# Kernel tuning notes

Measured on AMD Instinct MI355X. Metric: run time of the kernel, lower is better.

The kernel has to match this reference:

```python
import jax, jax.numpy as jnp
import numpy as np

D_MODEL, D_STATE, D_CONV, EXPAND = 1024, 16, 4, 2
D_INNER = EXPAND * D_MODEL
DT_RANK = (D_MODEL + 15) // 16  # 64
B_SZ, SEQ = 2, 1024


def _mamba_dir(x, inW, convW, convB, xpW, dtW, dtB, Alog, Dp, outW):
    """Standard Mamba block forward. x: [B, L, d_model]."""
    Bsz, L, _ = x.shape
    d_inner, d_state = Alog.shape
    dt_rank = xpW.shape[0] - 2 * d_state
    xz = jnp.einsum('bld,ed->ble', x, inW)            # [B, L, 2*d_inner]
    xi, z = jnp.split(xz, 2, axis=-1)
    # depthwise causal conv along L
    xc = jnp.swapaxes(xi, 1, 2)                       # [B, d_inner, L]
    xc = jax.lax.conv_general_dilated(
        xc, convW, window_strides=(1,),
        padding=[(convW.shape[-1] - 1, 0)],
        feature_group_count=d_inner)
    xc = xc + convB[None, :, None]
    u = jax.nn.silu(jnp.swapaxes(xc, 1, 2))           # [B, L, d_inner]
    x_dbl = jnp.einsum('bld,ed->ble', u, xpW)         # [B, L, dt_rank+2N]
    dt, Bm, Cm = jnp.split(x_dbl, [dt_rank, dt_rank + d_state], axis=-1)
    delta = jax.nn.softplus(jnp.einsum('blr,dr->bld', dt, dtW) + dtB)  # [B,L,d_inner]
    A = -jnp.exp(Alog)                                # [d_inner, d_state]

    def step(h, ins):
        d_t, B_t, C_t, u_t = ins                      # [B,D],[B,N],[B,N],[B,D]
        dA = jnp.exp(d_t[:, :, None] * A)             # [B, D, N]
        h = h * dA + (d_t * u_t)[:, :, None] * B_t[:, None, :]
        y_t = jnp.einsum('bdn,bn->bd', h, C_t)
        return h, y_t

    h0 = jnp.zeros((Bsz, d_inner, d_state), x.dtype)
    xs = (jnp.swapaxes(delta, 0, 1), jnp.swapaxes(Bm, 0, 1),
          jnp.swapaxes(Cm, 0, 1), jnp.swapaxes(u, 0, 1))
    _, ys = jax.lax.scan(step, h0, xs)
    y = jnp.swapaxes(ys, 0, 1)                        # [B, L, d_inner]
    y = y + u * Dp
    y = y * jax.nn.silu(z)
    return jnp.einsum('bld,od->blo', y, outW)         # [B, L, d_model]


def _make_params(key, suffix):
    ks = jax.random.split(key, 10)
    s = 0.02
    p = {
        'inW' + suffix: jax.random.normal(ks[0], (2 * D_INNER, D_MODEL), jnp.float32) * s,
        'convW' + suffix: jax.random.normal(ks[1], (D_INNER, 1, D_CONV), jnp.float32) * s,
        'convB' + suffix: jnp.zeros((D_INNER,), jnp.float32),
        'xpW' + suffix: jax.random.normal(ks[2], (DT_RANK + 2 * D_STATE, D_INNER), jnp.float32) * s,
        'dtW' + suffix: jax.random.normal(ks[3], (D_INNER, DT_RANK), jnp.float32) * s,
        'dtB' + suffix: jax.random.normal(ks[4], (D_INNER,), jnp.float32) * 0.1 - 4.0,
        'Alog' + suffix: jnp.log(1.0 + jax.random.uniform(ks[5], (D_INNER, D_STATE), jnp.float32) * 15.0),
        'Dp' + suffix: jnp.ones((D_INNER,), jnp.float32),
        'outW' + suffix: jax.random.normal(ks[6], (D_MODEL, D_INNER), jnp.float32) * s,
    }
    return p


def setup_inputs() -> dict:
    key = jax.random.key(0)
    kx, kf, kb = jax.random.split(key, 3)
    inp = {'x': jax.random.normal(kx, (B_SZ, SEQ, D_MODEL), jnp.float32)}
    inp.update(_make_params(kf, '_f'))
    inp.update(_make_params(kb, '_b'))
    return inp


def reference(x, inW_f, convW_f, convB_f, xpW_f, dtW_f, dtB_f, Alog_f, Dp_f, outW_f,
              inW_b, convW_b, convB_b, xpW_b, dtW_b, dtB_b, Alog_b, Dp_b, outW_b):
    y_fwd = _mamba_dir(x, inW_f, convW_f, convB_f, xpW_f, dtW_f, dtB_f, Alog_f, Dp_f, outW_f)
    xb = jnp.flip(x, axis=1)
    y_bwd = jnp.flip(_mamba_dir(xb, inW_b, convW_b, convB_b, xpW_b, dtW_b, dtB_b, Alog_b, Dp_b, outW_b), axis=1)
    return 0.5 * (y_fwd + y_bwd)
```

## Files before the change

kernel.cpp:

```cpp
#include <hip/hip_runtime.h>
#include <math.h>

#define B_SZ 2
#define SEQ  1024
#define DM   1024
#define DI   2048
#define NST  16
#define RNK  64
#define XPD  96
#define M_TOT (B_SZ*SEQ)
#define NC   32
#define LC   (SEQ/NC)
#define NCH  65536

typedef unsigned short ushort_t;
typedef __attribute__((ext_vector_type(8))) short short8;
typedef __attribute__((ext_vector_type(4))) float f32x4;

#if __has_builtin(__builtin_amdgcn_exp2f)
#define EXP2F __builtin_amdgcn_exp2f
#else
#define EXP2F exp2f
#endif
#define LOG2E 1.44269504f

__device__ __forceinline__ ushort_t f2bf(float f) {
    unsigned u = __float_as_uint(f);
    u += 0x7fff + ((u >> 16) & 1);
    return (ushort_t)(u >> 16);
}
__device__ __forceinline__ float bf2f(ushort_t v) {
    return __uint_as_float(((unsigned)v) << 16);
}

__global__ __launch_bounds__(256)
void f32_to_bf16(const float* __restrict__ in, ushort_t* __restrict__ out)
{
    int i = blockIdx.x * 256 + threadIdx.x;
    float4 v = ((const float4*)in)[i];
    ushort4 o;
    o.x = f2bf(v.x); o.y = f2bf(v.y); o.z = f2bf(v.z); o.w = f2bf(v.w);
    ((ushort4*)out)[i] = o;
}

__global__ __launch_bounds__(256)
void convert_all(const float* __restrict__ x,
                 const float* __restrict__ inWf, const float* __restrict__ inWb,
                 const float* __restrict__ outWf, const float* __restrict__ outWb,
                 ushort_t* __restrict__ xbf, ushort_t* __restrict__ inWcat,
                 ushort_t* __restrict__ outWcat)
{
    int bid = blockIdx.x;
    const float* src; ushort_t* dst; int rel; int strided = 0;
    if (bid < 2048)       { rel = bid;         src = x;     dst = xbf; }
    else if (bid < 6144)  { rel = bid - 2048;  src = inWf;  dst = inWcat; }
    else if (bid < 10240) { rel = bid - 6144;  src = inWb;  dst = inWcat + (size_t)2 * DI * DM; }
    else if (bid < 12288) { rel = bid - 10240; src = outWf; dst = outWcat;      strided = 1; }
    else                  { rel = bid - 12288; src = outWb; dst = outWcat + DI; strided = 1; }
    int i = rel * 256 + threadIdx.x;
    float4 v = ((const float4*)src)[i];
    ushort4 o;
    o.x = f2bf(v.x); o.y = f2bf(v.y); o.z = f2bf(v.z); o.w = f2bf(v.w);
    if (!strided) {
        ((ushort4*)dst)[i] = o;
    } else {
        int row = i >> 9;
        int c4  = (i - (row << 9)) << 2;
        *(ushort4*)(dst + (size_t)row * (2 * DI) + c4) = o;
    }
}

__device__ __forceinline__ void load_lds16(const ushort_t* g, ushort_t* l) {
    __builtin_amdgcn_global_load_lds(
        (const __attribute__((address_space(1))) void*)g,
        (__attribute__((address_space(3))) void*)l, 16, 0, 0);
}

template<bool OUT_BF16>
__global__ __launch_bounds__(256)
void gemm_gll(const ushort_t* __restrict__ A, const ushort_t* __restrict__ W,
              void* __restrict__ D, int M, int N, int K, int kLen, int ldD)
{
    __shared__ __align__(16) ushort_t As[128 * 64];
    __shared__ __align__(16) ushort_t Ws[128 * 64];
    const int t    = threadIdx.x;
    const int lane = t & 63;
    const int wave = t >> 6;
    const int wr   = (wave >> 1) * 64;
    const int wc   = (wave & 1) * 64;

    const int m0 = blockIdx.y * 128;
    const int n0 = blockIdx.x * 128;
    const int kStart = blockIdx.z * kLen;

    const int srow   = lane >> 3;
    const int gchunk = (lane & 7) ^ srow;

    f32x4 acc[4][4] = {};

    for (int k0 = kStart; k0 < kStart + kLen; k0 += 64) {
#pragma unroll
        for (int it = 0; it < 4; it++) {
            const int rb = wave * 32 + it * 8;
            load_lds16(A + (size_t)(m0 + rb + srow) * K + k0 + gchunk * 8,
                       As + rb * 64);
            load_lds16(W + (size_t)(n0 + rb + srow) * K + k0 + gchunk * 8,
                       Ws + rb * 64);
        }
        __syncthreads();
#pragma unroll
        for (int kk = 0; kk < 2; kk++) {
            const int kc = kk * 4 + (lane >> 4);
            short8 af[4], bf[4];
#pragma unroll
            for (int i = 0; i < 4; i++) {
                int r = wr + i * 16 + (lane & 15);
                af[i] = *(const short8*)(As + r * 64 + ((kc ^ (r & 7)) << 3));
            }
#pragma unroll
            for (int j = 0; j < 4; j++) {
                int r = wc + j * 16 + (lane & 15);
                bf[j] = *(const short8*)(Ws + r * 64 + ((kc ^ (r & 7)) << 3));
            }
#pragma unroll
            for (int i = 0; i < 4; i++)
#pragma unroll
                for (int j = 0; j < 4; j++)
                    acc[i][j] = __builtin_amdgcn_mfma_f32_16x16x32_bf16(
                        af[i], bf[j], acc[i][j], 0, 0, 0);
        }
        __syncthreads();
    }

    if (OUT_BF16) {
        ushort_t* Dp = (ushort_t*)D;
#pragma unroll
        for (int i = 0; i < 4; i++)
#pragma unroll
            for (int r = 0; r < 4; r++) {
                int m = m0 + wr + i * 16 + ((lane >> 4) << 2) + r;
#pragma unroll
                for (int j = 0; j < 4; j++) {
                    int n = n0 + wc + j * 16 + (lane & 15);
                    Dp[(size_t)m * ldD + n] = f2bf(acc[i][j][r]);
                }
            }
    } else {
        float* Dp = (float*)D + (size_t)blockIdx.z * M * ldD;
#pragma unroll
        for (int i = 0; i < 4; i++)
#pragma unroll
            for (int r = 0; r < 4; r++) {
                int m = m0 + wr + i * 16 + ((lane >> 4) << 2) + r;
#pragma unroll
                for (int j = 0; j < 4; j++) {
                    int n = n0 + wc + j * 16 + (lane & 15);
                    Dp[(size_t)m * ldD + n] = acc[i][j][r];
                }
            }
    }
}

__global__ __launch_bounds__(256)
void reduce4(const float* __restrict__ P, float* __restrict__ out)
{
    int i = blockIdx.x * 256 + threadIdx.x;
    const size_t S = (size_t)M_TOT * DM / 4;
    float4 a = ((const float4*)P)[i];
    float4 b = ((const float4*)P)[i + S];
    float4 c = ((const float4*)P)[i + 2 * S];
    float4 d = ((const float4*)P)[i + 3 * S];
    float4 o;
    o.x = 0.5f * (a.x + b.x + c.x + d.x);
    o.y = 0.5f * (a.y + b.y + c.y + d.y);
    o.z = 0.5f * (a.z + b.z + c.z + d.z);
    o.w = 0.5f * (a.w + b.w + c.w + d.w);
    ((float4*)out)[i] = o;
}

#define LDSP 72

__global__ __launch_bounds__(256)
void gemm2_splitk(const ushort_t* __restrict__ A, const ushort_t* __restrict__ W,
                  float* __restrict__ P, int M, int N, int K, int kLen)
{
    __shared__ __align__(16) ushort_t As[64 * LDSP];
    __shared__ __align__(16) ushort_t Ws[64 * LDSP];
    const int t    = threadIdx.x;
    const int lane = t & 63;
    const int wave = t >> 6;
    const int wr   = (wave >> 1) * 32;
    const int wc   = (wave & 1) * 32;

    f32x4 acc[2][2] = {};

    const int m0 = blockIdx.y * 64;
    const int n0 = blockIdx.x * 64;
    const int kStart = blockIdx.z * kLen;
    const int srow = t >> 3;
    const int scol = (t & 7) << 3;

    for (int k0 = kStart; k0 < kStart + kLen; k0 += 64) {
        {
            int r = srow;
            short8 v = *(const short8*)(A + (size_t)(m0 + r) * K + k0 + scol);
            *(short8*)(&As[r * LDSP + scol]) = v;
            int r2 = 32 + srow;
            short8 v2 = *(const short8*)(A + (size_t)(m0 + r2) * K + k0 + scol);
            *(short8*)(&As[r2 * LDSP + scol]) = v2;
            int wn = n0 + r;
            short8 wv = {};
            if (wn < N) wv = *(const short8*)(W + (size_t)wn * K + k0 + scol);
            *(short8*)(&Ws[r * LDSP + scol]) = wv;
            int wn2 = n0 + r2;
            short8 wv2 = {};
            if (wn2 < N) wv2 = *(const short8*)(W + (size_t)wn2 * K + k0 + scol);
            *(short8*)(&Ws[r2 * LDSP + scol]) = wv2;
        }
        __syncthreads();
#pragma unroll
        for (int kk = 0; kk < 2; kk++) {
            const int kcol = kk * 32 + ((lane >> 4) << 3);
            short8 af[2], bfr[2];
#pragma unroll
            for (int i = 0; i < 2; i++)
                af[i] = *(const short8*)(&As[(wr + i * 16 + (lane & 15)) * LDSP + kcol]);
#pragma unroll
            for (int j = 0; j < 2; j++)
                bfr[j] = *(const short8*)(&Ws[(wc + j * 16 + (lane & 15)) * LDSP + kcol]);
#pragma unroll
            for (int i = 0; i < 2; i++)
#pragma unroll
                for (int j = 0; j < 2; j++)
                    acc[i][j] = __builtin_amdgcn_mfma_f32_16x16x32_bf16(
                        af[i], bfr[j], acc[i][j], 0, 0, 0);
        }
        __syncthreads();
    }

    float* Pz = P + (size_t)blockIdx.z * M * XPD;
#pragma unroll
    for (int i = 0; i < 2; i++)
#pragma unroll
        for (int r = 0; r < 4; r++) {
            int m = m0 + wr + i * 16 + ((lane >> 4) << 2) + r;
#pragma unroll
            for (int j = 0; j < 2; j++) {
                int n = n0 + wc + j * 16 + (lane & 15);
                if (n < N) Pz[(size_t)m * XPD + n] = acc[i][j][r];
            }
        }
}

__global__ __launch_bounds__(256)
void xdbl_reduce(const float* __restrict__ P, float* __restrict__ xdbl)
{
    int i = blockIdx.x * 256 + threadIdx.x;
    const size_t S = (size_t)M_TOT * XPD / 4;
    float4 s = ((const float4*)P)[i];
#pragma unroll
    for (int z = 1; z < 8; z++) {
        float4 v = ((const float4*)P)[i + z * S];
        s.x += v.x; s.y += v.y; s.z += v.z; s.w += v.w;
    }
    ((float4*)xdbl)[i] = s;
}

__global__ __launch_bounds__(256)
void delta_gemm(const float* __restrict__ xdbl, const float* __restrict__ dtW,
                const float* __restrict__ dtB, float* __restrict__ delta)
{
    __shared__ __align__(16) ushort_t As[64 * LDSP];
    __shared__ __align__(16) ushort_t Ws[64 * LDSP];
    const int t    = threadIdx.x;
    const int lane = t & 63;
    const int wave = t >> 6;
    const int wr   = (wave >> 1) * 32;
    const int wc   = (wave & 1) * 32;

    const int m0 = blockIdx.y * 64;
    const int n0 = blockIdx.x * 64;
    const int srow = t >> 2;
    const int scol = (t & 3) << 4;

    {
        const float* ap = xdbl + (size_t)(m0 + srow) * XPD + scol;
        const float* wp = dtW  + (size_t)(n0 + srow) * RNK + scol;
        float4 a[4], w[4];
#pragma unroll
        for (int q = 0; q < 4; q++) { a[q] = ((const float4*)ap)[q]; w[q] = ((const float4*)wp)[q]; }
        __align__(16) ushort_t at[16], wt[16];
#pragma unroll
        for (int q = 0; q < 16; q++) {
            at[q] = f2bf(((const float*)a)[q]);
            wt[q] = f2bf(((const float*)w)[q]);
        }
        *(short8*)(&As[srow * LDSP + scol])     = *(const short8*)(at);
        *(short8*)(&As[srow * LDSP + scol + 8]) = *(const short8*)(at + 8);
        *(short8*)(&Ws[srow * LDSP + scol])     = *(const short8*)(wt);
        *(short8*)(&Ws[srow * LDSP + scol + 8]) = *(const short8*)(wt + 8);
    }
    __syncthreads();

    f32x4 acc[2][2] = {};
#pragma unroll
    for (int kk = 0; kk < 2; kk++) {
        const int kcol = kk * 32 + ((lane >> 4) << 3);
        short8 af[2], bfr[2];
#pragma unroll
        for (int i = 0; i < 2; i++)
            af[i] = *(const short8*)(&As[(wr + i * 16 + (lane & 15)) * LDSP + kcol]);
#pragma unroll
        for (int j = 0; j < 2; j++)
            bfr[j] = *(const short8*)(&Ws[(wc + j * 16 + (lane & 15)) * LDSP + kcol]);
#pragma unroll
        for (int i = 0; i < 2; i++)
#pragma unroll
            for (int j = 0; j < 2; j++)
                acc[i][j] = __builtin_amdgcn_mfma_f32_16x16x32_bf16(
                    af[i], bfr[j], acc[i][j], 0, 0, 0);
    }

#pragma unroll
    for (int j = 0; j < 2; j++) {
        int n = n0 + wc + j * 16 + (lane & 15);
        float bn = dtB[n];
#pragma unroll
        for (int i = 0; i < 2; i++) {
#pragma unroll
            for (int r = 0; r < 4; r++) {
                int m = m0 + wr + i * 16 + ((lane >> 4) << 2) + r;
                float v = acc[i][j][r] + bn;
                float sp = (v > 20.f) ? v : log1pf(__expf(v));
                delta[(size_t)m * DI + n] = sp;
            }
        }
    }
}

__global__ __launch_bounds__(256)
void conv_silu(const ushort_t* __restrict__ xzall, const float* __restrict__ convW,
               const float* __restrict__ convB, ushort_t* __restrict__ ubf, int dir)
{
    int idx = blockIdx.x * 256 + threadIdx.x;
    int di  = (idx & (DI / 4 - 1)) << 2;
    int m   = idx >> 9;
    int b   = m >> 10, l = m & (SEQ - 1);
    const ushort_t* xb = xzall + (size_t)b * SEQ * (4 * DI) + dir * (2 * DI) + di;

    float wv[4][4];
#pragma unroll
    for (int c = 0; c < 4; c++) {
        float4 w = *(const float4*)(convW + (di + c) * 4);
        wv[c][0] = w.x; wv[c][1] = w.y; wv[c][2] = w.z; wv[c][3] = w.w;
    }
    float4 cb = *(const float4*)(convB + di);
    float acc[4] = {cb.x, cb.y, cb.z, cb.w};
#pragma unroll
    for (int j = 0; j < 4; j++) {
        int srcl = dir ? (l + 3 - j) : (l - 3 + j);
        if ((unsigned)srcl < SEQ) {
            ushort4 xv = *(const ushort4*)(xb + (size_t)srcl * (4 * DI));
            acc[0] += wv[0][j] * bf2f(xv.x);
            acc[1] += wv[1][j] * bf2f(xv.y);
            acc[2] += wv[2][j] * bf2f(xv.z);
            acc[3] += wv[3][j] * bf2f(xv.w);
        }
    }
    ushort4 o;
    o.x = f2bf(acc[0] / (1.f + __expf(-acc[0])));
    o.y = f2bf(acc[1] / (1.f + __expf(-acc[1])));
    o.z = f2bf(acc[2] / (1.f + __expf(-acc[2])));
    o.w = f2bf(acc[3] / (1.f + __expf(-acc[3])));
    *(ushort4*)(ubf + (size_t)m * DI + di) = o;
}

__global__ __launch_bounds__(256)
void scan_pass1(const float* __restrict__ delta, const ushort_t* __restrict__ ubf,
                const float* __restrict__ xdbl, const float* __restrict__ Alog,
                float* __restrict__ Sb, float* __restrict__ SD, int dir)
{
    int tid = threadIdx.x, lane = tid & 63, wv = tid >> 6;
    int blk = blockIdx.x;
    int dg = blk & 7;
    int bc = blk >> 3;
    int c  = bc & (NC - 1);
    int b  = bc >> 5;
    int d  = (dg * 4 + wv) * 64 + lane;
    int t0 = dir ? (SEQ - 1 - c * LC) : (c * LC);
    int rs = dir ? -1 : 1;

    float ac2[NST];
#pragma unroll
    for (int q = 0; q < 4; q++) {
        float4 al = *(const float4*)(Alog + (size_t)d * NST + q * 4);
        ac2[q * 4 + 0] = -__expf(al.x) * LOG2E;
        ac2[q * 4 + 1] = -__expf(al.y) * LOG2E;
        ac2[q * 4 + 2] = -__expf(al.z) * LOG2E;
        ac2[q * 4 + 3] = -__expf(al.w) * LOG2E;
    }
    float h[NST];
#pragma unroll
    for (int n = 0; n < NST; n++) h[n] = 0.f;
    float sumD = 0.f;

#pragma unroll 4
    for (int l = 0; l < LC; l++) {
        int t = t0 + rs * l;
        size_t row = (size_t)b * SEQ + t;
        float dl = delta[row * DI + d];
        float uv = bf2f(ubf[row * DI + d]);
        const float* xr = xdbl + row * XPD + RNK;
        float4 Bv[4];
#pragma unroll
        for (int q = 0; q < 4; q++) Bv[q] = *(const float4*)(xr + q * 4);
        float dlu = dl * uv;
        sumD += dl;
#pragma unroll
        for (int n = 0; n < NST; n++) {
            float dA = EXP2F(dl * ac2[n]);
            h[n] = h[n] * dA + dlu * ((const float*)Bv)[n];
        }
    }

    size_t o = (size_t)c * NCH + ((size_t)b * DI + d) * NST;
#pragma unroll
    for (int q = 0; q < 4; q++)
        *(float4*)(Sb + o + q * 4) = make_float4(h[q*4], h[q*4+1], h[q*4+2], h[q*4+3]);
    SD[(size_t)c * (B_SZ * DI) + b * DI + d] = sumD;
}

__global__ __launch_bounds__(256)
void scan_combine(float* __restrict__ Sb, const float* __restrict__ SD,
                  const float* __restrict__ Alog)
{
    int i = blockIdx.x * 256 + threadIdx.x;
    int n = i & 15;
    int d = (i >> 4) & (DI - 1);
    int b = i >> 15;
    float ac2 = -__expf(Alog[(size_t)d * NST + n]) * LOG2E;
    float h = 0.f;
#pragma unroll
    for (int c = 0; c < NC; c++) {
        float s = Sb[(size_t)c * NCH + i];
        float p = EXP2F(ac2 * SD[(size_t)c * (B_SZ * DI) + b * DI + d]);
        Sb[(size_t)c * NCH + i] = h;
        h = s + p * h;
    }
}

__global__ __launch_bounds__(256)
void scan_pass2(const float* __restrict__ delta, const ushort_t* __restrict__ ubf,
                const float* __restrict__ xdbl, const ushort_t* __restrict__ xzall,
                const float* __restrict__ Alog, const float* __restrict__ Dp,
                const float* __restrict__ Hinit, ushort_t* __restrict__ ybf, int dir)
{
    int tid = threadIdx.x, lane = tid & 63, wv = tid >> 6;
    int blk = blockIdx.x;
    int dg = blk & 7;
    int bc = blk >> 3;
    int c  = bc & (NC - 1);
    int b  = bc >> 5;
    int d  = (dg * 4 + wv) * 64 + lane;
    int t0 = dir ? (SEQ - 1 - c * LC) : (c * LC);
    int rs = dir ? -1 : 1;

    float ac2[NST];
#pragma unroll
    for (int q = 0; q < 4; q++) {
        float4 al = *(const float4*)(Alog + (size_t)d * NST + q * 4);
        ac2[q * 4 + 0] = -__expf(al.x) * LOG2E;
        ac2[q * 4 + 1] = -__expf(al.y) * LOG2E;
        ac2[q * 4 + 2] = -__expf(al.z) * LOG2E;
        ac2[q * 4 + 3] = -__expf(al.w) * LOG2E;
    }
    float dp = Dp[d];
    float h[NST];
    {
        size_t o = (size_t)c * NCH + ((size_t)b * DI + d) * NST;
#pragma unroll
        for (int q = 0; q < 4; q++) {
            float4 hv = *(const float4*)(Hinit + o + q * 4);
            h[q*4] = hv.x; h[q*4+1] = hv.y; h[q*4+2] = hv.z; h[q*4+3] = hv.w;
        }
    }

#pragma unroll 4
    for (int l = 0; l < LC; l++) {
        int t = t0 + rs * l;
        size_t row = (size_t)b * SEQ + t;
        float dl = delta[row * DI + d];
        float uv = bf2f(ubf[row * DI + d]);
        const float* xr = xdbl + row * XPD + RNK;
        float4 Bv[4], Cv[4];
#pragma unroll
        for (int q = 0; q < 4; q++) {
            Bv[q] = *(const float4*)(xr + q * 4);
            Cv[q] = *(const float4*)(xr + NST + q * 4);
        }
        float dlu = dl * uv;
        float y = 0.f;
#pragma unroll
        for (int n = 0; n < NST; n++) {
            float dA = EXP2F(dl * ac2[n]);
            h[n] = h[n] * dA + dlu * ((const float*)Bv)[n];
            y += h[n] * ((const float*)Cv)[n];
        }
        float z = bf2f(xzall[row * (4 * DI) + dir * (2 * DI) + DI + d]);
        float yv = (y + uv * dp) * (z / (1.f + __expf(-z)));
        ybf[row * (2 * DI) + dir * DI + d] = f2bf(yv);
    }
}

extern "C" void kernel_launch(void* const* d_in, const int* in_sizes, int n_in,
                              void* d_out, int out_size, void* d_ws, size_t ws_size,
                              hipStream_t stream)
{
    char* wsb = (char*)d_ws;

    ushort_t* xzall  = (ushort_t*)wsb;
    float*    delta  = (float*)(wsb + 33554432);
    ushort_t* ubf    = (ushort_t*)(wsb + 50331648);
    ushort_t* ybf    = (ushort_t*)(wsb + 58720256);
    ushort_t* inWcat = (ushort_t*)(wsb + 75497472);
    ushort_t* outWcat= (ushort_t*)(wsb + 92274688);
    ushort_t* xbf    = (ushort_t*)(wsb + 100663296);

    float* Sb    = (float*)inWcat;
    float* part2 = (float*)(wsb + 75497472 + 8388608);
    float* xdbl  = (float*)(wsb + 90177536);
    float* SD    = (float*)(wsb + 90963968);
    ushort_t* xpWbf = xbf;
    float* part4 = (float*)xzall;

    float* out = (float*)d_out;
    dim3 blk(256);

    convert_all<<<14336, blk, 0, stream>>>(
        (const float*)d_in[0], (const float*)d_in[1], (const float*)d_in[10],
        (const float*)d_in[9], (const float*)d_in[18], xbf, inWcat, outWcat);

    gemm_gll<true><<<dim3(8192 / 128, M_TOT / 128, 1), blk, 0, stream>>>(
        xbf, inWcat, xzall, M_TOT, 8192, DM, DM, 8192);

    for (int dir = 0; dir < 2; dir++) {
        int pb = 1 + dir * 9;
        const float* convW = (const float*)d_in[pb + 1];
        const float* convB = (const float*)d_in[pb + 2];
        const float* xpW   = (const float*)d_in[pb + 3];
        const float* dtW   = (const float*)d_in[pb + 4];
        const float* dtB   = (const float*)d_in[pb + 5];
        const float* Alog  = (const float*)d_in[pb + 6];
        const float* Dp    = (const float*)d_in[pb + 7];

        f32_to_bf16<<<(XPD * DI) / 1024, blk, 0, stream>>>(xpW, xpWbf);

        conv_silu<<<(M_TOT * DI / 4) / 256, blk, 0, stream>>>(xzall, convW, convB,
                                                              ubf, dir);

        gemm2_splitk<<<dim3(2, M_TOT / 64, 8), blk, 0, stream>>>(
            ubf, xpWbf, part2, M_TOT, XPD, DI, DI / 8);
        xdbl_reduce<<<(M_TOT * XPD / 4) / 256, blk, 0, stream>>>(part2, xdbl);

        delta_gemm<<<dim3(DI / 64, M_TOT / 64), blk, 0, stream>>>(xdbl, dtW, dtB,
                                                                  delta);

        scan_pass1<<<B_SZ * NC * 8, blk, 0, stream>>>(delta, ubf, xdbl, Alog,
                                                      Sb, SD, dir);
        scan_combine<<<NCH / 256, blk, 0, stream>>>(Sb, SD, Alog);
        scan_pass2<<<B_SZ * NC * 8, blk, 0, stream>>>(delta, ubf, xdbl, xzall,
                                                      Alog, Dp, Sb, ybf, dir);
    }

    gemm_gll<false><<<dim3(DM / 128, M_TOT / 128, 4), blk, 0, stream>>>(
        ybf, outWcat, part4, M_TOT, DM, 2 * DI, DI / 2, DM);
    reduce4<<<(M_TOT * DM / 4) / 256, blk, 0, stream>>>(part4, out);
}
```

Before: 413.0 us.

## Batch both scan directions into single launches and store delta as bf16

Merges the forward and backward direction pipelines so that each stage (conv+silu, x-projection split-K GEMM, reduce, delta GEMM, scan passes, combine) runs once over both directions, with the direction taken from the grid index. The xpW conversion moves into the one-time convert kernel, and delta is now stored as bf16 instead of fp32. The aim is fewer kernel launches, better grid occupancy for the small scan kernels, and less memory traffic for delta. In exchange the workspace is reorganised and bf16 rounding of delta adds precision error to the scan.

```diff
diff --git a/kernel.cpp b/kernel.cpp
--- a/kernel.cpp
+++ b/kernel.cpp
@@ -34,21 +34,12 @@
 }
 
 __global__ __launch_bounds__(256)
-void f32_to_bf16(const float* __restrict__ in, ushort_t* __restrict__ out)
-{
-    int i = blockIdx.x * 256 + threadIdx.x;
-    float4 v = ((const float4*)in)[i];
-    ushort4 o;
-    o.x = f2bf(v.x); o.y = f2bf(v.y); o.z = f2bf(v.z); o.w = f2bf(v.w);
-    ((ushort4*)out)[i] = o;
-}
-
-__global__ __launch_bounds__(256)
 void convert_all(const float* __restrict__ x,
                  const float* __restrict__ inWf, const float* __restrict__ inWb,
                  const float* __restrict__ outWf, const float* __restrict__ outWb,
+                 const float* __restrict__ xpWf, const float* __restrict__ xpWb,
                  ushort_t* __restrict__ xbf, ushort_t* __restrict__ inWcat,
-                 ushort_t* __restrict__ outWcat)
+                 ushort_t* __restrict__ outWcat, ushort_t* __restrict__ xpWcat)
 {
     int bid = blockIdx.x;
     const float* src; ushort_t* dst; int rel; int strided = 0;
@@ -56,7 +47,9 @@
     else if (bid < 6144)  { rel = bid - 2048;  src = inWf;  dst = inWcat; }
     else if (bid < 10240) { rel = bid - 6144;  src = inWb;  dst = inWcat + (size_t)2 * DI * DM; }
     else if (bid < 12288) { rel = bid - 10240; src = outWf; dst = outWcat;      strided = 1; }
-    else                  { rel = bid - 12288; src = outWb; dst = outWcat + DI; strided = 1; }
+    else if (bid < 14336) { rel = bid - 12288; src = outWb; dst = outWcat + DI; strided = 1; }
+    else if (bid < 14528) { rel = bid - 14336; src = xpWf;  dst = xpWcat; }
+    else                  { rel = bid - 14528; src = xpWb;  dst = xpWcat + (size_t)XPD * DI; }
     int i = rel * 256 + threadIdx.x;
     float4 v = ((const float4*)src)[i];
     ushort4 o;
@@ -181,9 +174,15 @@
 #define LDSP 72
 
 __global__ __launch_bounds__(256)
-void gemm2_splitk(const ushort_t* __restrict__ A, const ushort_t* __restrict__ W,
-                  float* __restrict__ P, int M, int N, int K, int kLen)
-{
+void gemm2_splitk2(const ushort_t* __restrict__ ubf, const ushort_t* __restrict__ xpWcat,
+                   float* __restrict__ P)
+{
+    const int dir = blockIdx.z >> 3;
+    const int kz  = blockIdx.z & 7;
+    const ushort_t* A = ubf + (size_t)dir * M_TOT * DI;
+    const ushort_t* W = xpWcat + (size_t)dir * XPD * DI;
+    const int K = DI, N = XPD;
+
     __shared__ __align__(16) ushort_t As[64 * LDSP];
     __shared__ __align__(16) ushort_t Ws[64 * LDSP];
     const int t    = threadIdx.x;
@@ -196,11 +195,11 @@
 
     const int m0 = blockIdx.y * 64;
     const int n0 = blockIdx.x * 64;
-    const int kStart = blockIdx.z * kLen;
+    const int kStart = kz * (DI / 8);
     const int srow = t >> 3;
     const int scol = (t & 7) << 3;
 
-    for (int k0 = kStart; k0 < kStart + kLen; k0 += 64) {
+    for (int k0 = kStart; k0 < kStart + DI / 8; k0 += 64) {
         {
             int r = srow;
             short8 v = *(const short8*)(A + (size_t)(m0 + r) * K + k0 + scol);
@@ -238,7 +237,7 @@
         __syncthreads();
     }
 
-    float* Pz = P + (size_t)blockIdx.z * M * XPD;
+    float* Pz = P + ((size_t)dir * 8 + kz) * M_TOT * XPD;
 #pragma unroll
     for (int i = 0; i < 2; i++)
 #pragma unroll
@@ -253,23 +252,34 @@
 }
 
 __global__ __launch_bounds__(256)
-void xdbl_reduce(const float* __restrict__ P, float* __restrict__ xdbl)
-{
-    int i = blockIdx.x * 256 + threadIdx.x;
+void xdbl_reduce2(const float* __restrict__ P, float* __restrict__ xdbl)
+{
+    int bid = blockIdx.x;
+    int dir = bid >= 192;
+    int i = (bid - dir * 192) * 256 + threadIdx.x;
     const size_t S = (size_t)M_TOT * XPD / 4;
-    float4 s = ((const float4*)P)[i];
+    const float4* Pd = (const float4*)(P + (size_t)dir * 8 * M_TOT * XPD);
+    float4 s = Pd[i];
 #pragma unroll
     for (int z = 1; z < 8; z++) {
-        float4 v = ((const float4*)P)[i + z * S];
+        float4 v = Pd[i + z * S];
         s.x += v.x; s.y += v.y; s.z += v.z; s.w += v.w;
     }
-    ((float4*)xdbl)[i] = s;
-}
-
-__global__ __launch_bounds__(256)
-void delta_gemm(const float* __restrict__ xdbl, const float* __restrict__ dtW,
-                const float* __restrict__ dtB, float* __restrict__ delta)
-{
+    ((float4*)(xdbl + (size_t)dir * M_TOT * XPD))[i] = s;
+}
+
+__global__ __launch_bounds__(256)
+void delta_gemm2(const float* __restrict__ xdbl,
+                 const float* __restrict__ dtWf, const float* __restrict__ dtWb,
+                 const float* __restrict__ dtBf, const float* __restrict__ dtBb,
+                 ushort_t* __restrict__ deltab)
+{
+    const int dir = blockIdx.z;
+    const float* xd  = xdbl + (size_t)dir * M_TOT * XPD;
+    const float* dtW = dir ? dtWb : dtWf;
+    const float* dtB = dir ? dtBb : dtBf;
+    ushort_t* delta  = deltab + (size_t)dir * M_TOT * DI;
+
     __shared__ __align__(16) ushort_t As[64 * LDSP];
     __shared__ __align__(16) ushort_t Ws[64 * LDSP];
     const int t    = threadIdx.x;
@@ -284,8 +294,8 @@
     const int scol = (t & 3) << 4;
 
     {
-        const float* ap = xdbl + (size_t)(m0 + srow) * XPD + scol;
-        const float* wp = dtW  + (size_t)(n0 + srow) * RNK + scol;
+        const float* ap = xd  + (size_t)(m0 + srow) * XPD + scol;
+        const float* wp = dtW + (size_t)(n0 + srow) * RNK + scol;
         float4 a[4], w[4];
 #pragma unroll
         for (int q = 0; q < 4; q++) { a[q] = ((const float4*)ap)[q]; w[q] = ((const float4*)wp)[q]; }
@@ -332,17 +342,23 @@
                 int m = m0 + wr + i * 16 + ((lane >> 4) << 2) + r;
                 float v = acc[i][j][r] + bn;
                 float sp = (v > 20.f) ? v : log1pf(__expf(v));
-                delta[(size_t)m * DI + n] = sp;
+                delta[(size_t)m * DI + n] = f2bf(sp);
             }
         }
     }
 }
 
 __global__ __launch_bounds__(256)
-void conv_silu(const ushort_t* __restrict__ xzall, const float* __restrict__ convW,
-               const float* __restrict__ convB, ushort_t* __restrict__ ubf, int dir)
-{
-    int idx = blockIdx.x * 256 + threadIdx.x;
+void conv_silu2(const ushort_t* __restrict__ xzall,
+                const float* __restrict__ convWf, const float* __restrict__ convWb,
+                const float* __restrict__ convBf, const float* __restrict__ convBb,
+                ushort_t* __restrict__ ubf)
+{
+    int bid = blockIdx.x;
+    int dir = bid >> 12;
+    int idx = (bid & 4095) * 256 + threadIdx.x;
+    const float* convW = dir ? convWb : convWf;
+    const float* convB = dir ? convBb : convBf;
     int di  = (idx & (DI / 4 - 1)) << 2;
     int m   = idx >> 9;
     int b   = m >> 10, l = m & (SEQ - 1);
@@ -372,16 +388,19 @@
     o.y = f2bf(acc[1] / (1.f + __expf(-acc[1])));
     o.z = f2bf(acc[2] / (1.f + __expf(-acc[2])));
     o.w = f2bf(acc[3] / (1.f + __expf(-acc[3])));
-    *(ushort4*)(ubf + (size_t)m * DI + di) = o;
-}
-
-__global__ __launch_bounds__(256)
-void scan_pass1(const float* __restrict__ delta, const ushort_t* __restrict__ ubf,
-                const float* __restrict__ xdbl, const float* __restrict__ Alog,
-                float* __restrict__ Sb, float* __restrict__ SD, int dir)
+    *(ushort4*)(ubf + (size_t)dir * M_TOT * DI + (size_t)m * DI + di) = o;
+}
+
+__global__ __launch_bounds__(256)
+void scan_pass1_2(const ushort_t* __restrict__ deltab, const ushort_t* __restrict__ ubf,
+                  const float* __restrict__ xdbl,
+                  const float* __restrict__ Alogf, const float* __restrict__ Alogb,
+                  float* __restrict__ Sb, float* __restrict__ SD)
 {
     int tid = threadIdx.x, lane = tid & 63, wv = tid >> 6;
     int blk = blockIdx.x;
+    int dir = blk >> 9;
+    blk &= 511;
     int dg = blk & 7;
     int bc = blk >> 3;
     int c  = bc & (NC - 1);
@@ -390,6 +409,13 @@
     int t0 = dir ? (SEQ - 1 - c * LC) : (c * LC);
     int rs = dir ? -1 : 1;
 
+    const float* Alog = dir ? Alogb : Alogf;
+    const ushort_t* dl_p = deltab + (size_t)dir * M_TOT * DI;
+    const ushort_t* u_p  = ubf    + (size_t)dir * M_TOT * DI;
+    const float*    xd   = xdbl   + (size_t)dir * M_TOT * XPD;
+    float* Sbd = Sb + (size_t)dir * NC * NCH;
+    float* SDd = SD + (size_t)dir * NC * B_SZ * DI;
+
     float ac2[NST];
 #pragma unroll
     for (int q = 0; q < 4; q++) {
@@ -408,9 +434,9 @@
     for (int l = 0; l < LC; l++) {
         int t = t0 + rs * l;
         size_t row = (size_t)b * SEQ + t;
-        float dl = delta[row * DI + d];
-        float uv = bf2f(ubf[row * DI + d]);
-        const float* xr = xdbl + row * XPD + RNK;
+        float dl = bf2f(dl_p[row * DI + d]);
+        float uv = bf2f(u_p[row * DI + d]);
+        const float* xr = xd + row * XPD + RNK;
         float4 Bv[4];
 #pragma unroll
         for (int q = 0; q < 4; q++) Bv[q] = *(const float4*)(xr + q * 4);
@@ -426,37 +452,45 @@
     size_t o = (size_t)c * NCH + ((size_t)b * DI + d) * NST;
 #pragma unroll
     for (int q = 0; q < 4; q++)
-        *(float4*)(Sb + o + q * 4) = make_float4(h[q*4], h[q*4+1], h[q*4+2], h[q*4+3]);
-    SD[(size_t)c * (B_SZ * DI) + b * DI + d] = sumD;
-}
-
-__global__ __launch_bounds__(256)
-void scan_combine(float* __restrict__ Sb, const float* __restrict__ SD,
-                  const float* __restrict__ Alog)
-{
-    int i = blockIdx.x * 256 + threadIdx.x;
+        *(float4*)(Sbd + o + q * 4) = make_float4(h[q*4], h[q*4+1], h[q*4+2], h[q*4+3]);
+    SDd[(size_t)c * (B_SZ * DI) + b * DI + d] = sumD;
+}
+
+__global__ __launch_bounds__(256)
+void scan_combine2(float* __restrict__ Sb, const float* __restrict__ SD,
+                   const float* __restrict__ Alogf, const float* __restrict__ Alogb)
+{
+    int gid = blockIdx.x * 256 + threadIdx.x;
+    int dir = gid >= NCH;
+    int i = gid - dir * NCH;
     int n = i & 15;
     int d = (i >> 4) & (DI - 1);
     int b = i >> 15;
+    const float* Alog = dir ? Alogb : Alogf;
+    float* Sbd = Sb + (size_t)dir * NC * NCH;
+    const float* SDd = SD + (size_t)dir * NC * B_SZ * DI;
     float ac2 = -__expf(Alog[(size_t)d * NST + n]) * LOG2E;
     float h = 0.f;
 #pragma unroll
     for (int c = 0; c < NC; c++) {
-        float s = Sb[(size_t)c * NCH + i];
-        float p = EXP2F(ac2 * SD[(size_t)c * (B_SZ * DI) + b * DI + d]);
-        Sb[(size_t)c * NCH + i] = h;
+        float s = Sbd[(size_t)c * NCH + i];
+        float p = EXP2F(ac2 * SDd[(size_t)c * (B_SZ * DI) + b * DI + d]);
+        Sbd[(size_t)c * NCH + i] = h;
         h = s + p * h;
     }
 }
 
 __global__ __launch_bounds__(256)
-void scan_pass2(const float* __restrict__ delta, const ushort_t* __restrict__ ubf,
-                const float* __restrict__ xdbl, const ushort_t* __restrict__ xzall,
-                const float* __restrict__ Alog, const float* __restrict__ Dp,
-                const float* __restrict__ Hinit, ushort_t* __restrict__ ybf, int dir)
+void scan_pass2_2(const ushort_t* __restrict__ deltab, const ushort_t* __restrict__ ubf,
+                  const float* __restrict__ xdbl, const ushort_t* __restrict__ xzall,
+                  const float* __restrict__ Alogf, const float* __restrict__ Alogb,
+                  const float* __restrict__ Dpf, const float* __restrict__ Dpb,
+                  const float* __restrict__ Hinit, ushort_t* __restrict__ ybf)
 {
     int tid = threadIdx.x, lane = tid & 63, wv = tid >> 6;
     int blk = blockIdx.x;
+    int dir = blk >> 9;
+    blk &= 511;
     int dg = blk & 7;
     int bc = blk >> 3;
     int c  = bc & (NC - 1);
@@ -465,6 +499,13 @@
     int t0 = dir ? (SEQ - 1 - c * LC) : (c * LC);
     int rs = dir ? -1 : 1;
 
+    const float* Alog = dir ? Alogb : Alogf;
+    const float* Dpp  = dir ? Dpb : Dpf;
+    const ushort_t* dl_p = deltab + (size_t)dir * M_TOT * DI;
+    const ushort_t* u_p  = ubf    + (size_t)dir * M_TOT * DI;
+    const float*    xd   = xdbl   + (size_t)dir * M_TOT * XPD;
+    const float*    Hin  = Hinit  + (size_t)dir * NC * NCH;
+
     float ac2[NST];
 #pragma unroll
     for (int q = 0; q < 4; q++) {
@@ -474,13 +515,13 @@
         ac2[q * 4 + 2] = -__expf(al.z) * LOG2E;
         ac2[q * 4 + 3] = -__expf(al.w) * LOG2E;
     }
-    float dp = Dp[d];
+    float dp = Dpp[d];
     float h[NST];
     {
         size_t o = (size_t)c * NCH + ((size_t)b * DI + d) * NST;
 #pragma unroll
         for (int q = 0; q < 4; q++) {
-            float4 hv = *(const float4*)(Hinit + o + q * 4);
+            float4 hv = *(const float4*)(Hin + o + q * 4);
             h[q*4] = hv.x; h[q*4+1] = hv.y; h[q*4+2] = hv.z; h[q*4+3] = hv.w;
         }
     }
@@ -489,9 +530,9 @@
     for (int l = 0; l < LC; l++) {
         int t = t0 + rs * l;
         size_t row = (size_t)b * SEQ + t;
-        float dl = delta[row * DI + d];
-        float uv = bf2f(ubf[row * DI + d]);
-        const float* xr = xdbl + row * XPD + RNK;
+        float dl = bf2f(dl_p[row * DI + d]);
+        float uv = bf2f(u_p[row * DI + d]);
+        const float* xr = xd + row * XPD + RNK;
         float4 Bv[4], Cv[4];
 #pragma unroll
         for (int q = 0; q < 4; q++) {
@@ -519,60 +560,54 @@
     char* wsb = (char*)d_ws;
 
     ushort_t* xzall  = (ushort_t*)wsb;
-    float*    delta  = (float*)(wsb + 33554432);
-    ushort_t* ubf    = (ushort_t*)(wsb + 50331648);
-    ushort_t* ybf    = (ushort_t*)(wsb + 58720256);
-    ushort_t* inWcat = (ushort_t*)(wsb + 75497472);
-    ushort_t* outWcat= (ushort_t*)(wsb + 92274688);
-    ushort_t* xbf    = (ushort_t*)(wsb + 100663296);
+    ushort_t* ybf    = (ushort_t*)(wsb + 33554432);
+    ushort_t* inWcat = (ushort_t*)(wsb + 50331648);
+    ushort_t* outWcat= (ushort_t*)(wsb + 67108864);
+    ushort_t* xbf    = (ushort_t*)(wsb + 75497472);
+    ushort_t* xpWcat = (ushort_t*)(wsb + 79691776);
+    ushort_t* ubf    = (ushort_t*)(wsb + 80478208);
+    ushort_t* deltab = (ushort_t*)(wsb + 97255424);
+    float*    xdbl   = (float*)(wsb + 114032640);
 
     float* Sb    = (float*)inWcat;
-    float* part2 = (float*)(wsb + 75497472 + 8388608);
-    float* xdbl  = (float*)(wsb + 90177536);
-    float* SD    = (float*)(wsb + 90963968);
-    ushort_t* xpWbf = xbf;
+    float* SD    = (float*)xbf;
+    float* part2 = (float*)deltab;
     float* part4 = (float*)xzall;
 
     float* out = (float*)d_out;
     dim3 blk(256);
 
-    convert_all<<<14336, blk, 0, stream>>>(
+    convert_all<<<14720, blk, 0, stream>>>(
         (const float*)d_in[0], (const float*)d_in[1], (const float*)d_in[10],
-        (const float*)d_in[9], (const float*)d_in[18], xbf, inWcat, outWcat);
+        (const float*)d_in[9], (const float*)d_in[18],
+        (const float*)d_in[4], (const float*)d_in[13],
+        xbf, inWcat, outWcat, xpWcat);
 
     gemm_gll<true><<<dim3(8192 / 128, M_TOT / 128, 1), blk, 0, stream>>>(
         xbf, inWcat, xzall, M_TOT, 8192, DM, DM, 8192);
 
-    for (int dir = 0; dir < 2; dir++) {
-        int pb = 1 + dir * 9;
-        const float* convW = (const float*)d_in[pb + 1];
-        const float* convB = (const float*)d_in[pb + 2];
-        const float* xpW   = (const float*)d_in[pb + 3];
-        const float* dtW   = (const float*)d_in[pb + 4];
-        const float* dtB   = (const float*)d_in[pb + 5];
-        const float* Alog  = (const float*)d_in[pb + 6];
-        const float* Dp    = (const float*)d_in[pb + 7];
-
-        f32_to_bf16<<<(XPD * DI) / 1024, blk, 0, stream>>>(xpW, xpWbf);
-
-        conv_silu<<<(M_TOT * DI / 4) / 256, blk, 0, stream>>>(xzall, convW, convB,
-                                                              ubf, dir);
-
-        gemm2_splitk<<<dim3(2, M_TOT / 64, 8), blk, 0, stream>>>(
-            ubf, xpWbf, part2, M_TOT, XPD, DI, DI / 8);
-        xdbl_reduce<<<(M_TOT * XPD / 4) / 256, blk, 0, stream>>>(part2, xdbl);
-
-        delta_gemm<<<dim3(DI / 64, M_TOT / 64), blk, 0, stream>>>(xdbl, dtW, dtB,
-                                                                  delta);
-
-        scan_pass1<<<B_SZ * NC * 8, blk, 0, stream>>>(delta, ubf, xdbl, Alog,
-                                                      Sb, SD, dir);
-        scan_combine<<<NCH / 256, blk, 0, stream>>>(Sb, SD, Alog);
-        scan_pass2<<<B_SZ * NC * 8, blk, 0, stream>>>(delta, ubf, xdbl, xzall,
-                                                      Alog, Dp, Sb, ybf, dir);
-    }
+    conv_silu2<<<8192, blk, 0, stream>>>(xzall,
+        (const float*)d_in[2], (const float*)d_in[11],
+        (const float*)d_in[3], (const float*)d_in[12], ubf);
+
+    gemm2_splitk2<<<dim3(2, M_TOT / 64, 16), blk, 0, stream>>>(ubf, xpWcat, part2);
+
+    xdbl_reduce2<<<384, blk, 0, stream>>>(part2, xdbl);
+
+    delta_gemm2<<<dim3(DI / 64, M_TOT / 64, 2), blk, 0, stream>>>(
+        xdbl, (const float*)d_in[5], (const float*)d_in[14],
+        (const float*)d_in[6], (const float*)d_in[15], deltab);
+
+    scan_pass1_2<<<1024, blk, 0, stream>>>(deltab, ubf, xdbl,
+        (const float*)d_in[7], (const float*)d_in[16], Sb, SD);
+    scan_combine2<<<2 * NCH / 256, blk, 0, stream>>>(Sb, SD,
+        (const float*)d_in[7], (const float*)d_in[16]);
+    scan_pass2_2<<<1024, blk, 0, stream>>>(deltab, ubf, xdbl, xzall,
+        (const float*)d_in[7], (const float*)d_in[16],
+        (const float*)d_in[8], (const float*)d_in[17], Sb, ybf);
 
     gemm_gll<false><<<dim3(DM / 128, M_TOT / 128, 4), blk, 0, stream>>>(
         ybf, outWcat, part4, M_TOT, DM, 2 * DI, DI / 2, DM);
+
     reduce4<<<(M_TOT * DM / 4) / 256, blk, 0, stream>>>(part4, out);
 }
```

After: 357.8 us. 13.4% less time.
